# Optimization experiments

Measured on AMD Instinct MI355X. Metric: run time of the kernel, lower is better.

Reference implementation:

```python
import jax, jax.numpy as jnp
import numpy as np

DIM = 1024
NUM_HEAD = 16
DIM_HEAD = DIM // NUM_HEAD
RMS_EPS = 1.1920929e-07  # torch.finfo(float32).eps (nn.RMSNorm default eps=None)
EPS_LIN = 1e-6
THETA = 10000.0


def rmsnorm(x, g, eps=RMS_EPS):
    return x * jax.lax.rsqrt(jnp.mean(x * x, axis=-1, keepdims=True) + eps) * g


def rope_cos_sin(seq_len, dim_head, dtype=jnp.float32):
    inv_freq = 1.0 / (THETA ** (jnp.arange(0, dim_head, 2, dtype=dtype) / dim_head))
    t = jnp.arange(seq_len, dtype=dtype)
    freqs = jnp.outer(t, inv_freq)  # [L, dh//2]
    return jnp.cos(freqs), jnp.sin(freqs)


def apply_rope(t, cos, sin):
    # t: [b, h, L, dh]; pairs are (t[...,2i], t[...,2i+1]) viewed as complex
    tr = t[..., 0::2]
    ti = t[..., 1::2]
    out_r = tr * cos - ti * sin
    out_i = tr * sin + ti * cos
    return jnp.stack([out_r, out_i], axis=-1).reshape(t.shape)


def setup_inputs() -> dict:
    key = jax.random.key(0)
    ks = jax.random.split(key, 5)
    B, L = 4, 4096
    x = jax.random.normal(ks[0], (B, L, DIM), dtype=jnp.float32)
    Wqkv = jax.random.normal(ks[1], (3 * DIM, DIM), dtype=jnp.float32) * 0.02
    bqkv = jax.random.normal(ks[2], (3 * DIM,), dtype=jnp.float32) * 0.02
    gq = jnp.ones((DIM,), dtype=jnp.float32)
    gk = jnp.ones((DIM,), dtype=jnp.float32)
    Wout = jax.random.normal(ks[3], (DIM, DIM), dtype=jnp.float32) * 0.02
    bout = jax.random.normal(ks[4], (DIM,), dtype=jnp.float32) * 0.02
    gout = jnp.ones((DIM,), dtype=jnp.float32)
    return {"x": x, "Wqkv": Wqkv, "bqkv": bqkv, "gq": gq, "gk": gk,
            "Wout": Wout, "bout": bout, "gout": gout}


def reference(x, Wqkv, bqkv, gq, gk, Wout, bout, gout):
    B, L, D = x.shape
    qkv = x @ Wqkv.T + bqkv  # [B, L, 3D]
    q, k, v = jnp.split(qkv, 3, axis=-1)
    q = rmsnorm(q, gq)
    k = rmsnorm(k, gk)
    # b L (h d) -> b h L d
    split = lambda t: t.reshape(B, L, NUM_HEAD, DIM_HEAD).transpose(0, 2, 1, 3)
    q, k, v = split(q), split(k), split(v)
    cos, sin = rope_cos_sin(L, DIM_HEAD)  # start_pos = 0 (default)
    cos = cos[None, None]  # [1,1,L,dh//2]
    sin = sin[None, None]
    q = apply_rope(q, cos, sin)
    k = apply_rope(k, cos, sin)
    # linear attention: ReLU feature map + padded-value normalization trick
    qf = jax.nn.relu(q)
    kf = jax.nn.relu(k)
    vpad = jnp.concatenate([v, jnp.ones_like(v[..., :1])], axis=-1)  # pad_val=1.0
    vk = jnp.einsum('bhlp,bhld->bhpd', vpad, kf)       # [b,h,dh+1,dh]
    res = jnp.einsum('bhpd,bhld->bhlp', vk, qf)        # [b,h,L,dh+1]
    attn = res[..., :-1] / (res[..., -1:] + EPS_LIN)
    attn = attn.transpose(0, 2, 1, 3).reshape(B, L, D)  # b h L d -> b L (h d)
    out = rmsnorm(attn @ Wout.T + bout, gout)
    return out
```

## Files before the change

kernel.cpp:

```cpp
#include <hip/hip_runtime.h>
#include <stdint.h>

#define RMS_EPS 1.1920929e-07f
#define EPS_LIN 1e-6f

typedef __attribute__((ext_vector_type(8))) short bf16x8;
typedef __attribute__((ext_vector_type(4))) float f32x4;

__device__ __forceinline__ unsigned short f2bf(float f) {
  union { float f; unsigned int u; } v; v.f = f;
  unsigned int r = v.u + 0x7fffu + ((v.u >> 16) & 1u);
  return (unsigned short)(r >> 16);
}
__device__ __forceinline__ float bf2f(unsigned short s) {
  union { unsigned int u; float f; } v; v.u = ((unsigned int)s) << 16;
  return v.f;
}

__global__ __launch_bounds__(256) void k_init(
    const float* __restrict__ x, const float* __restrict__ Wqkv,
    const float* __restrict__ Wout,
    unsigned short* __restrict__ xb, unsigned short* __restrict__ wqkvb,
    unsigned short* __restrict__ woutb,
    float* __restrict__ cosT, float* __restrict__ sinT) {
  const int blk = blockIdx.x;
  const int t = threadIdx.x;
  if (blk < 20480) {
    const float* src;
    unsigned short* dst;
    int base;
    if (blk < 16384) { src = x; dst = xb; base = blk; }
    else if (blk < 19456) { src = Wqkv; dst = wqkvb; base = blk - 16384; }
    else { src = Wout; dst = woutb; base = blk - 19456; }
    int i = (base * 256 + t) * 4;
    float4 v = *reinterpret_cast<const float4*>(src + i);
    ushort4 o = { f2bf(v.x), f2bf(v.y), f2bf(v.z), f2bf(v.w) };
    *reinterpret_cast<ushort4*>(dst + i) = o;
  } else {
    int idx = (blk - 20480) * 256 + t;
    int l = idx >> 5, i = idx & 31;
    float inv_freq = expf(-((float)(2 * i) / 64.0f) * logf(10000.0f));
    float ang = (float)l * inv_freq;
    cosT[idx] = cosf(ang);
    sinT[idx] = sinf(ang);
  }
}

__device__ __forceinline__ void stage16(const unsigned short* g, unsigned short* lds_base,
                                        int lane) {
#if __has_builtin(__builtin_amdgcn_global_load_lds)
  __builtin_amdgcn_global_load_lds(
      (const __attribute__((address_space(1))) unsigned int*)g,
      (__attribute__((address_space(3))) unsigned int*)lds_base, 16, 0, 0);
#else
  *reinterpret_cast<uint4*>(lds_base + lane * 8) = *reinterpret_cast<const uint4*>(g);
#endif
}

__global__ __launch_bounds__(256, 3) void k_gemm_bt(
    const unsigned short* __restrict__ A, const unsigned short* __restrict__ Bw,
    const float* __restrict__ bias, int M, int N, int K, int mode,
    unsigned short* __restrict__ qb, unsigned short* __restrict__ kb,
    unsigned short* __restrict__ vb, unsigned short* __restrict__ preb) {
  __shared__ unsigned short As[128 * 64];
  __shared__ unsigned short Bs[128 * 64];
  const int nt = N >> 7;
  const int nwg = gridDim.x;
  const int wg = (blockIdx.x & 7) * (nwg >> 3) + (blockIdx.x >> 3);
  int ksplit = 0, tile = wg;
  if (mode == 1) { ksplit = wg >> 10; tile = wg & 1023; }
  const int bm = tile / nt, bn = tile % nt;
  const int m0 = bm << 7, n0 = bn << 7;
  const int kbeg = (mode == 1) ? (ksplit << 9) : 0;
  const int kend = (mode == 1) ? (kbeg + 512) : K;
  const int t = threadIdx.x;
  const int wave = t >> 6, lane = t & 63;
  const int wr = wave >> 1, wc = wave & 1;
  const int quad = lane >> 4, m16 = lane & 15;

  const unsigned short* ApS[4];
  const unsigned short* BpS[4];
  unsigned short* AlS[4];
  unsigned short* BlS[4];
#pragma unroll
  for (int s = 0; s < 4; ++s) {
    int u = wave * 256 + s * 64 + lane;
    int row = u >> 3;
    int ku = (u & 7) ^ (row & 7);
    ApS[s] = A + (size_t)(m0 + row) * K + ku * 8;
    BpS[s] = Bw + (size_t)(n0 + row) * K + ku * 8;
    AlS[s] = As + (size_t)(wave * 256 + s * 64) * 8;
    BlS[s] = Bs + (size_t)(wave * 256 + s * 64) * 8;
  }

  int offA[4][2], offB[4][2];
#pragma unroll
  for (int i = 0; i < 4; ++i) {
    int rowA = wr * 64 + i * 16 + m16;
    int rowB = wc * 64 + i * 16 + m16;
#pragma unroll
    for (int ks = 0; ks < 2; ++ks) {
      int kuf = ks * 4 + quad;
      offA[i][ks] = (rowA * 8 + (kuf ^ (rowA & 7))) * 8;
      offB[i][ks] = (rowB * 8 + (kuf ^ (rowB & 7))) * 8;
    }
  }

  f32x4 acc[4][4] = {};

  for (int k0 = kbeg; k0 < kend; k0 += 64) {
#pragma unroll
    for (int s = 0; s < 4; ++s) {
      stage16(ApS[s] + k0, AlS[s], lane);
      stage16(BpS[s] + k0, BlS[s], lane);
    }
    __syncthreads();
#pragma unroll
    for (int ks = 0; ks < 2; ++ks) {
      bf16x8 fa[4], fb[4];
#pragma unroll
      for (int i = 0; i < 4; ++i)
        fa[i] = *reinterpret_cast<const bf16x8*>(As + offA[i][ks]);
#pragma unroll
      for (int j = 0; j < 4; ++j)
        fb[j] = *reinterpret_cast<const bf16x8*>(Bs + offB[j][ks]);
#pragma unroll
      for (int i = 0; i < 4; ++i)
#pragma unroll
        for (int j = 0; j < 4; ++j)
          acc[i][j] = __builtin_amdgcn_mfma_f32_16x16x32_bf16(fa[i], fb[j], acc[i][j], 0, 0, 0);
    }
    __syncthreads();
  }

  unsigned short* po = preb + (size_t)ksplit * 16777216ull;
#pragma unroll
  for (int i = 0; i < 4; ++i) {
    int rbase = m0 + wr * 64 + i * 16 + quad * 4;
#pragma unroll
    for (int j = 0; j < 4; ++j) {
      int col = n0 + wc * 64 + j * 16 + m16;
      float bc = (mode == 0 || ksplit == 0) ? bias[col] : 0.f;
#pragma unroll
      for (int r = 0; r < 4; ++r) {
        int row = rbase + r;
        float val = acc[i][j][r] + bc;
        unsigned short bv = f2bf(val);
        if (mode == 0) {
          if (col < 1024) {
            qb[(size_t)row * 1024 + col] = bv;
          } else if (col < 2048) {
            kb[(size_t)row * 1024 + (col - 1024)] = bv;
          } else {
            int h = (col - 2048) >> 6, d = col & 63;
            int b = row >> 12, l = row & 4095;
            vb[(((size_t)(b * 16 + h)) * 4096 + l) * 64 + d] = bv;
          }
        } else {
          po[(size_t)row * N + col] = bv;
        }
      }
    }
  }
}

__global__ __launch_bounds__(256) void k_qknorm(
    const unsigned short* __restrict__ qb, const unsigned short* __restrict__ kb,
    const float* __restrict__ gq, const float* __restrict__ gk,
    const float* __restrict__ cosT, const float* __restrict__ sinT,
    unsigned short* __restrict__ qfb, unsigned short* __restrict__ kfb) {
  const int wid = (blockIdx.x << 2) + (threadIdx.x >> 6);
  const int row = wid >> 1;
  const int which = wid & 1;
  const int lane = threadIdx.x & 63;
  const int l = row & 4095;
  const int b = row >> 12;
  const unsigned short* src = (which ? kb : qb) + (size_t)row * 1024 + lane * 16;
  const float* g = which ? gk : gq;
  unsigned short* dstb = which ? kfb : qfb;

  bf16x8 u0 = *reinterpret_cast<const bf16x8*>(src);
  bf16x8 u1 = *reinterpret_cast<const bf16x8*>(src + 8);
  float v[16];
  float ss = 0.f;
#pragma unroll
  for (int e = 0; e < 8; ++e) {
    v[e] = bf2f((unsigned short)u0[e]);
    v[8 + e] = bf2f((unsigned short)u1[e]);
  }
#pragma unroll
  for (int e = 0; e < 16; ++e) ss += v[e] * v[e];
#pragma unroll
  for (int off = 1; off < 64; off <<= 1) ss += __shfl_xor(ss, off, 64);
  const float sc = rsqrtf(ss * (1.0f / 1024.0f) + RMS_EPS);

  const float* gp = g + lane * 16;
  const float* cp = cosT + l * 32 + (lane & 3) * 8;
  const float* sp = sinT + l * 32 + (lane & 3) * 8;
  bf16x8 o0, o1;
#pragma unroll
  for (int p = 0; p < 8; ++p) {
    float cc = cp[p], sv = sp[p];
    float x0 = v[2 * p] * sc * gp[2 * p];
    float x1 = v[2 * p + 1] * sc * gp[2 * p + 1];
    float r0 = x0 * cc - x1 * sv;
    float r1 = x0 * sv + x1 * cc;
    unsigned short b0 = f2bf(fmaxf(r0, 0.f));
    unsigned short b1 = f2bf(fmaxf(r1, 0.f));
    if (p < 4) { o0[2 * p] = (short)b0; o0[2 * p + 1] = (short)b1; }
    else { o1[2 * (p - 4)] = (short)b0; o1[2 * (p - 4) + 1] = (short)b1; }
  }
  unsigned short* dp =
      dstb + (((size_t)(b * 16 + (lane >> 2))) * 4096 + l) * 64 + (lane & 3) * 16;
  *reinterpret_cast<bf16x8*>(dp) = o0;
  *reinterpret_cast<bf16x8*>(dp + 8) = o1;
}

__global__ __launch_bounds__(256) void k_vk(const unsigned short* __restrict__ vb,
                                            const unsigned short* __restrict__ kfb,
                                            float* __restrict__ part) {
  const int bh = blockIdx.x >> 4;
  const int chunk = blockIdx.x & 15;
  const int t = threadIdx.x;
  const int wv = t >> 6, lane = t & 63;
  const int quad = lane >> 4, m16 = lane & 15;

  __shared__ __align__(16) unsigned short Vt[64 * 40];
  __shared__ __align__(16) unsigned short Kt[64 * 40];
  __shared__ float dred[4][64];

  f32x4 acc[4] = {};
  float accD = 0.f;

  for (int tile = 0; tile < 8; ++tile) {
    const size_t rbase =
        ((size_t)bh * 4096 + chunk * 256 + tile * 32 + wv * 8) * 64 + lane;
    bf16x8 vv, kv;
#pragma unroll
    for (int j = 0; j < 8; ++j) {
      unsigned short ve = vb[rbase + j * 64];
      unsigned short ke = kfb[rbase + j * 64];
      vv[j] = (short)ve;
      kv[j] = (short)ke;
      accD += bf2f(ke);
    }
    *reinterpret_cast<bf16x8*>(Vt + lane * 40 + wv * 8) = vv;
    *reinterpret_cast<bf16x8*>(Kt + lane * 40 + wv * 8) = kv;
    __syncthreads();

    bf16x8 fa = *reinterpret_cast<const bf16x8*>(Vt + (wv * 16 + m16) * 40 + quad * 8);
#pragma unroll
    for (int j = 0; j < 4; ++j) {
      bf16x8 fb = *reinterpret_cast<const bf16x8*>(Kt + (j * 16 + m16) * 40 + quad * 8);
      acc[j] = __builtin_amdgcn_mfma_f32_16x16x32_bf16(fa, fb, acc[j], 0, 0, 0);
    }
    __syncthreads();
  }

  float* dst = part + ((size_t)chunk * 64 + bh) * 4160;
#pragma unroll
  for (int j = 0; j < 4; ++j)
#pragma unroll
    for (int r = 0; r < 4; ++r)
      dst[(wv * 16 + quad * 4 + r) * 64 + j * 16 + m16] = acc[j][r];

  dred[wv][lane] = accD;
  __syncthreads();
  if (t < 64) dst[64 * 64 + t] = dred[0][t] + dred[1][t] + dred[2][t] + dred[3][t];
}

__global__ __launch_bounds__(256) void k_vkred(const float* __restrict__ part,
                                               float* __restrict__ vk) {
  const int i = (blockIdx.x * 256 + threadIdx.x) * 4;
  float4 s = *reinterpret_cast<const float4*>(part + i);
#pragma unroll
  for (int c = 1; c < 16; ++c) {
    float4 r = *reinterpret_cast<const float4*>(part + (size_t)c * 266240 + i);
    s.x += r.x; s.y += r.y; s.z += r.z; s.w += r.w;
  }
  *reinterpret_cast<float4*>(vk + i) = s;
}

__global__ __launch_bounds__(256) void k_res(const unsigned short* __restrict__ qfb,
                                             const float* __restrict__ vk,
                                             unsigned short* __restrict__ attnb) {
  const int bh = blockIdx.x >> 5;
  const int lt = (blockIdx.x & 31) << 7;
  const int b = bh >> 4, h = bh & 15;
  const int t = threadIdx.x;
  const int wave = t >> 6, lane = t & 63;
  __shared__ unsigned short Aq[128 * 64];
  __shared__ unsigned short Bv[64 * 64];
  __shared__ float vkD[64];
  __shared__ float invden[128];

  const unsigned short* Ag = qfb + ((size_t)bh * 4096 + lt) * 64;
#pragma unroll
  for (int s = 0; s < 4; ++s)
    stage16(Ag + wave * 2048 + s * 512 + lane * 8, Aq + wave * 2048 + s * 512, lane);

  const float* vsrc = vk + (size_t)bh * 65 * 64;
  {
    int base = t * 16;
#pragma unroll
    for (int c = 0; c < 4; ++c) {
      float4 f = *reinterpret_cast<const float4*>(vsrc + base + c * 4);
      ushort4 o = { f2bf(f.x), f2bf(f.y), f2bf(f.z), f2bf(f.w) };
      *reinterpret_cast<ushort4*>(Bv + base + c * 4) = o;
    }
  }
  if (t < 64) vkD[t] = vsrc[64 * 64 + t];
  __syncthreads();

  f32x4 acc[2][4] = {};
  const int quad = lane >> 4, m16 = lane & 15;
#pragma unroll
  for (int step = 0; step < 2; ++step) {
    bf16x8 fa[2], fb[4];
#pragma unroll
    for (int i = 0; i < 2; ++i)
      fa[i] = *reinterpret_cast<const bf16x8*>(Aq + (wave * 32 + i * 16 + m16) * 64 +
                                               step * 32 + quad * 8);
#pragma unroll
    for (int j = 0; j < 4; ++j)
      fb[j] = *reinterpret_cast<const bf16x8*>(Bv + (j * 16 + m16) * 64 +
                                               step * 32 + quad * 8);
#pragma unroll
    for (int i = 0; i < 2; ++i)
#pragma unroll
      for (int j = 0; j < 4; ++j)
        acc[i][j] = __builtin_amdgcn_mfma_f32_16x16x32_bf16(fa[i], fb[j], acc[i][j], 0, 0, 0);
  }

  {
    const unsigned short* qr = Aq + (t >> 1) * 64 + (t & 1) * 32;
    const float* vd = vkD + (t & 1) * 32;
    float ds = 0.f;
#pragma unroll
    for (int c = 0; c < 4; ++c) {
      bf16x8 qv = *reinterpret_cast<const bf16x8*>(qr + c * 8);
#pragma unroll
      for (int j = 0; j < 8; ++j)
        ds += bf2f((unsigned short)qv[j]) * vd[c * 8 + j];
    }
    ds += __shfl_xor(ds, 1, 64);
    if ((t & 1) == 0) invden[t >> 1] = 1.0f / (ds + EPS_LIN);
  }
  __syncthreads();

#pragma unroll
  for (int i = 0; i < 2; ++i) {
#pragma unroll
    for (int r = 0; r < 4; ++r) {
      int row = wave * 32 + i * 16 + quad * 4 + r;
      float inv = invden[row];
      unsigned short* dst = attnb + ((size_t)(b * 4096 + lt + row)) * 1024 + h * 64;
#pragma unroll
      for (int j = 0; j < 4; ++j)
        dst[j * 16 + m16] = f2bf(acc[i][j][r] * inv);
    }
  }
}

__global__ __launch_bounds__(256) void k_outnorm(const unsigned short* __restrict__ preb0,
                                                 const unsigned short* __restrict__ preb1,
                                                 const float* __restrict__ gout,
                                                 float* __restrict__ out) {
  const int row = (blockIdx.x << 2) + (threadIdx.x >> 6);
  const int lane = threadIdx.x & 63;
  const unsigned short* s0 = preb0 + (size_t)row * 1024 + lane * 16;
  const unsigned short* s1 = preb1 + (size_t)row * 1024 + lane * 16;
  float* drow = out + (size_t)row * 1024 + lane * 16;
  bf16x8 a0 = *reinterpret_cast<const bf16x8*>(s0);
  bf16x8 a1 = *reinterpret_cast<const bf16x8*>(s0 + 8);
  bf16x8 b0 = *reinterpret_cast<const bf16x8*>(s1);
  bf16x8 b1 = *reinterpret_cast<const bf16x8*>(s1 + 8);
  float v[16];
  float ss = 0.f;
#pragma unroll
  for (int e = 0; e < 8; ++e) {
    v[e] = bf2f((unsigned short)a0[e]) + bf2f((unsigned short)b0[e]);
    v[8 + e] = bf2f((unsigned short)a1[e]) + bf2f((unsigned short)b1[e]);
  }
#pragma unroll
  for (int e = 0; e < 16; ++e) ss += v[e] * v[e];
#pragma unroll
  for (int off = 1; off < 64; off <<= 1) ss += __shfl_xor(ss, off, 64);
  const float sc = rsqrtf(ss * (1.0f / 1024.0f) + RMS_EPS);
  const float* gp = gout + lane * 16;
#pragma unroll
  for (int c = 0; c < 4; ++c) {
    float4 o = { v[c * 4 + 0] * sc * gp[c * 4 + 0], v[c * 4 + 1] * sc * gp[c * 4 + 1],
                 v[c * 4 + 2] * sc * gp[c * 4 + 2], v[c * 4 + 3] * sc * gp[c * 4 + 3] };
    *reinterpret_cast<float4*>(drow + c * 4) = o;
  }
}

#define OFF_XB     0ull
#define OFF_WQKVB  33554432ull
#define OFF_WOUTB  39845888ull
#define OFF_QB     41943040ull
#define OFF_KB     75497472ull
#define OFF_VB     109051904ull
#define OFF_QFB    142606336ull
#define OFF_KFB    176160768ull
#define OFF_VK     209715200ull
#define OFF_ATTNB  210780160ull
#define OFF_COST   244334592ull
#define OFF_SINT   244858880ull
#define WS_NEEDED  245383168ull

extern "C" void kernel_launch(void* const* d_in, const int* in_sizes, int n_in,
                              void* d_out, int out_size, void* d_ws, size_t ws_size,
                              hipStream_t stream) {
  const float* x    = (const float*)d_in[0];
  const float* Wqkv = (const float*)d_in[1];
  const float* bqkv = (const float*)d_in[2];
  const float* gq   = (const float*)d_in[3];
  const float* gk   = (const float*)d_in[4];
  const float* Wout = (const float*)d_in[5];
  const float* bout = (const float*)d_in[6];
  const float* gout = (const float*)d_in[7];

  if (ws_size < WS_NEEDED) return;

  char* ws = (char*)d_ws;
  unsigned short* xb    = (unsigned short*)(ws + OFF_XB);
  unsigned short* wqkvb = (unsigned short*)(ws + OFF_WQKVB);
  unsigned short* woutb = (unsigned short*)(ws + OFF_WOUTB);
  unsigned short* qb    = (unsigned short*)(ws + OFF_QB);
  unsigned short* kb    = (unsigned short*)(ws + OFF_KB);
  unsigned short* vb    = (unsigned short*)(ws + OFF_VB);
  unsigned short* qfb   = (unsigned short*)(ws + OFF_QFB);
  unsigned short* kfb   = (unsigned short*)(ws + OFF_KFB);
  float*          vkbuf = (float*)(ws + OFF_VK);
  unsigned short* attnb = (unsigned short*)(ws + OFF_ATTNB);
  float*          cosT  = (float*)(ws + OFF_COST);
  float*          sinT  = (float*)(ws + OFF_SINT);
  unsigned short* preb0 = (unsigned short*)(ws + OFF_QB);
  unsigned short* preb1 = (unsigned short*)(ws + OFF_KB);
  float*          vkpart = (float*)(ws + OFF_ATTNB);

  k_init<<<20992, 256, 0, stream>>>(x, Wqkv, Wout, xb, wqkvb, woutb, cosT, sinT);

  k_gemm_bt<<<128 * 24, 256, 0, stream>>>(xb, wqkvb, bqkv, 16384, 3072, 1024, 0,
                                          qb, kb, vb, nullptr);
  k_qknorm<<<8192, 256, 0, stream>>>(qb, kb, gq, gk, cosT, sinT, qfb, kfb);

  k_vk<<<1024, 256, 0, stream>>>(vb, kfb, vkpart);
  k_vkred<<<260, 256, 0, stream>>>(vkpart, vkbuf);

  k_res<<<2048, 256, 0, stream>>>(qfb, vkbuf, attnb);

  k_gemm_bt<<<2048, 256, 0, stream>>>(attnb, woutb, bout, 16384, 1024, 1024, 1,
                                      nullptr, nullptr, nullptr, preb0);
  k_outnorm<<<4096, 256, 0, stream>>>(preb0, preb1, gout, (float*)d_out);
}
```

Before: 386.1 us.

## Fuse x fp32-to-bf16 conversion into QKV GEMM and drop out-proj split-K

The QKV GEMM now reads x directly in fp32 and converts to bf16 while staging into LDS, removing the separate conversion pass over x and the bf16 copy it wrote. The output-projection GEMM drops its 2-way split-K, writing one pre-norm buffer, so the norm kernel reads one partial instead of summing two. The blockIdx swizzle for L2 locality is also removed. In exchange, the QKV GEMM does synchronous fp32 loads (twice the bytes) instead of async global_load_lds, and the out GEMM launches half as many workgroups.

After: 438.3 us. 1.14x slower.

```diff
diff --git a/kernel.cpp b/kernel.cpp
--- a/kernel.cpp
+++ b/kernel.cpp
@@ -18,26 +18,23 @@
 }
 
 __global__ __launch_bounds__(256) void k_init(
-    const float* __restrict__ x, const float* __restrict__ Wqkv,
-    const float* __restrict__ Wout,
-    unsigned short* __restrict__ xb, unsigned short* __restrict__ wqkvb,
-    unsigned short* __restrict__ woutb,
+    const float* __restrict__ Wqkv, const float* __restrict__ Wout,
+    unsigned short* __restrict__ wqkvb, unsigned short* __restrict__ woutb,
     float* __restrict__ cosT, float* __restrict__ sinT) {
   const int blk = blockIdx.x;
   const int t = threadIdx.x;
-  if (blk < 20480) {
+  if (blk < 4096) {
     const float* src;
     unsigned short* dst;
     int base;
-    if (blk < 16384) { src = x; dst = xb; base = blk; }
-    else if (blk < 19456) { src = Wqkv; dst = wqkvb; base = blk - 16384; }
-    else { src = Wout; dst = woutb; base = blk - 19456; }
+    if (blk < 3072) { src = Wqkv; dst = wqkvb; base = blk; }
+    else { src = Wout; dst = woutb; base = blk - 3072; }
     int i = (base * 256 + t) * 4;
     float4 v = *reinterpret_cast<const float4*>(src + i);
     ushort4 o = { f2bf(v.x), f2bf(v.y), f2bf(v.z), f2bf(v.w) };
     *reinterpret_cast<ushort4*>(dst + i) = o;
   } else {
-    int idx = (blk - 20480) * 256 + t;
+    int idx = (blk - 4096) * 256 + t;
     int l = idx >> 5, i = idx & 31;
     float inv_freq = expf(-((float)(2 * i) / 64.0f) * logf(10000.0f));
     float ang = (float)l * inv_freq;
@@ -58,26 +55,22 @@
 }
 
 __global__ __launch_bounds__(256, 3) void k_gemm_bt(
-    const unsigned short* __restrict__ A, const unsigned short* __restrict__ Bw,
+    const float* __restrict__ Af, const unsigned short* __restrict__ A,
+    const unsigned short* __restrict__ Bw,
     const float* __restrict__ bias, int M, int N, int K, int mode,
     unsigned short* __restrict__ qb, unsigned short* __restrict__ kb,
     unsigned short* __restrict__ vb, unsigned short* __restrict__ preb) {
   __shared__ unsigned short As[128 * 64];
   __shared__ unsigned short Bs[128 * 64];
   const int nt = N >> 7;
-  const int nwg = gridDim.x;
-  const int wg = (blockIdx.x & 7) * (nwg >> 3) + (blockIdx.x >> 3);
-  int ksplit = 0, tile = wg;
-  if (mode == 1) { ksplit = wg >> 10; tile = wg & 1023; }
-  const int bm = tile / nt, bn = tile % nt;
+  const int bm = blockIdx.x / nt, bn = blockIdx.x % nt;
   const int m0 = bm << 7, n0 = bn << 7;
-  const int kbeg = (mode == 1) ? (ksplit << 9) : 0;
-  const int kend = (mode == 1) ? (kbeg + 512) : K;
   const int t = threadIdx.x;
   const int wave = t >> 6, lane = t & 63;
   const int wr = wave >> 1, wc = wave & 1;
   const int quad = lane >> 4, m16 = lane & 15;
 
+  const float* AfS[4];
   const unsigned short* ApS[4];
   const unsigned short* BpS[4];
   unsigned short* AlS[4];
@@ -87,6 +80,7 @@
     int u = wave * 256 + s * 64 + lane;
     int row = u >> 3;
     int ku = (u & 7) ^ (row & 7);
+    AfS[s] = Af + (size_t)(m0 + row) * K + ku * 8;
     ApS[s] = A + (size_t)(m0 + row) * K + ku * 8;
     BpS[s] = Bw + (size_t)(n0 + row) * K + ku * 8;
     AlS[s] = As + (size_t)(wave * 256 + s * 64) * 8;
@@ -108,11 +102,27 @@
 
   f32x4 acc[4][4] = {};
 
-  for (int k0 = kbeg; k0 < kend; k0 += 64) {
-#pragma unroll
-    for (int s = 0; s < 4; ++s) {
-      stage16(ApS[s] + k0, AlS[s], lane);
-      stage16(BpS[s] + k0, BlS[s], lane);
+  for (int k0 = 0; k0 < K; k0 += 64) {
+    if (mode == 0) {
+#pragma unroll
+      for (int s = 0; s < 4; ++s) {
+        const float* p = AfS[s] + k0;
+        float4 f0 = *reinterpret_cast<const float4*>(p);
+        float4 f1 = *reinterpret_cast<const float4*>(p + 4);
+        bf16x8 o;
+        o[0] = (short)f2bf(f0.x); o[1] = (short)f2bf(f0.y);
+        o[2] = (short)f2bf(f0.z); o[3] = (short)f2bf(f0.w);
+        o[4] = (short)f2bf(f1.x); o[5] = (short)f2bf(f1.y);
+        o[6] = (short)f2bf(f1.z); o[7] = (short)f2bf(f1.w);
+        *reinterpret_cast<bf16x8*>(AlS[s] + lane * 8) = o;
+        stage16(BpS[s] + k0, BlS[s], lane);
+      }
+    } else {
+#pragma unroll
+      for (int s = 0; s < 4; ++s) {
+        stage16(ApS[s] + k0, AlS[s], lane);
+        stage16(BpS[s] + k0, BlS[s], lane);
+      }
     }
     __syncthreads();
 #pragma unroll
@@ -133,14 +143,13 @@
     __syncthreads();
   }
 
-  unsigned short* po = preb + (size_t)ksplit * 16777216ull;
 #pragma unroll
   for (int i = 0; i < 4; ++i) {
     int rbase = m0 + wr * 64 + i * 16 + quad * 4;
 #pragma unroll
     for (int j = 0; j < 4; ++j) {
       int col = n0 + wc * 64 + j * 16 + m16;
-      float bc = (mode == 0 || ksplit == 0) ? bias[col] : 0.f;
+      float bc = bias[col];
 #pragma unroll
       for (int r = 0; r < 4; ++r) {
         int row = rbase + r;
@@ -157,7 +166,7 @@
             vb[(((size_t)(b * 16 + h)) * 4096 + l) * 64 + d] = bv;
           }
         } else {
-          po[(size_t)row * N + col] = bv;
+          preb[(size_t)row * N + col] = bv;
         }
       }
     }
@@ -362,25 +371,21 @@
   }
 }
 
-__global__ __launch_bounds__(256) void k_outnorm(const unsigned short* __restrict__ preb0,
-                                                 const unsigned short* __restrict__ preb1,
+__global__ __launch_bounds__(256) void k_outnorm(const unsigned short* __restrict__ preb,
                                                  const float* __restrict__ gout,
                                                  float* __restrict__ out) {
   const int row = (blockIdx.x << 2) + (threadIdx.x >> 6);
   const int lane = threadIdx.x & 63;
-  const unsigned short* s0 = preb0 + (size_t)row * 1024 + lane * 16;
-  const unsigned short* s1 = preb1 + (size_t)row * 1024 + lane * 16;
+  const unsigned short* src = preb + (size_t)row * 1024 + lane * 16;
   float* drow = out + (size_t)row * 1024 + lane * 16;
-  bf16x8 a0 = *reinterpret_cast<const bf16x8*>(s0);
-  bf16x8 a1 = *reinterpret_cast<const bf16x8*>(s0 + 8);
-  bf16x8 b0 = *reinterpret_cast<const bf16x8*>(s1);
-  bf16x8 b1 = *reinterpret_cast<const bf16x8*>(s1 + 8);
+  bf16x8 a0 = *reinterpret_cast<const bf16x8*>(src);
+  bf16x8 a1 = *reinterpret_cast<const bf16x8*>(src + 8);
   float v[16];
   float ss = 0.f;
 #pragma unroll
   for (int e = 0; e < 8; ++e) {
-    v[e] = bf2f((unsigned short)a0[e]) + bf2f((unsigned short)b0[e]);
-    v[8 + e] = bf2f((unsigned short)a1[e]) + bf2f((unsigned short)b1[e]);
+    v[e] = bf2f((unsigned short)a0[e]);
+    v[8 + e] = bf2f((unsigned short)a1[e]);
   }
 #pragma unroll
   for (int e = 0; e < 16; ++e) ss += v[e] * v[e];
@@ -425,7 +430,6 @@
   if (ws_size < WS_NEEDED) return;
 
   char* ws = (char*)d_ws;
-  unsigned short* xb    = (unsigned short*)(ws + OFF_XB);
   unsigned short* wqkvb = (unsigned short*)(ws + OFF_WQKVB);
   unsigned short* woutb = (unsigned short*)(ws + OFF_WOUTB);
   unsigned short* qb    = (unsigned short*)(ws + OFF_QB);
@@ -437,13 +441,12 @@
   unsigned short* attnb = (unsigned short*)(ws + OFF_ATTNB);
   float*          cosT  = (float*)(ws + OFF_COST);
   float*          sinT  = (float*)(ws + OFF_SINT);
-  unsigned short* preb0 = (unsigned short*)(ws + OFF_QB);
-  unsigned short* preb1 = (unsigned short*)(ws + OFF_KB);
+  unsigned short* preb  = (unsigned short*)(ws + OFF_QB);
   float*          vkpart = (float*)(ws + OFF_ATTNB);
 
-  k_init<<<20992, 256, 0, stream>>>(x, Wqkv, Wout, xb, wqkvb, woutb, cosT, sinT);
-
-  k_gemm_bt<<<128 * 24, 256, 0, stream>>>(xb, wqkvb, bqkv, 16384, 3072, 1024, 0,
+  k_init<<<4608, 256, 0, stream>>>(Wqkv, Wout, wqkvb, woutb, cosT, sinT);
+
+  k_gemm_bt<<<128 * 24, 256, 0, stream>>>(x, nullptr, wqkvb, bqkv, 16384, 3072, 1024, 0,
                                           qb, kb, vb, nullptr);
   k_qknorm<<<8192, 256, 0, stream>>>(qb, kb, gq, gk, cosT, sinT, qfb, kfb);
 
@@ -452,7 +455,7 @@
 
   k_res<<<2048, 256, 0, stream>>>(qfb, vkbuf, attnb);
 
-  k_gemm_bt<<<2048, 256, 0, stream>>>(attnb, woutb, bout, 16384, 1024, 1024, 1,
-                                      nullptr, nullptr, nullptr, preb0);
-  k_outnorm<<<4096, 256, 0, stream>>>(preb0, preb1, gout, (float*)d_out);
-}
+  k_gemm_bt<<<128 * 8, 256, 0, stream>>>(nullptr, attnb, woutb, bout, 16384, 1024, 1024, 1,
+                                         nullptr, nullptr, nullptr, preb);
+  k_outnorm<<<4096, 256, 0, stream>>>(preb, gout, (float*)d_out);
+}
```

## Drop split-K in output GEMM, remove XCD swizzle, raise occupancy hint

Applied to the files above, without the earlier changes.

Removes the two-way split-K in the output projection GEMM, so each workgroup now computes the full K=1024 reduction and writes a single bf16 pre-norm buffer. The outnorm kernel then reads one partial instead of summing two. This drops a second 32MB bf16 partial write and read and one extra rounding step. In exchange the output GEMM launches only 1024 workgroups, fewer than before. The change also removes the XCD-aware block remapping and raises the launch_bounds occupancy hint from 3 to 4 waves per SIMD, which may restrict registers.

Result: faster. 374.1 us (median of 2 runs) (-3.1%).

```diff
diff --git a/kernel.cpp b/kernel.cpp
--- a/kernel.cpp
+++ b/kernel.cpp
@@ -57,7 +57,7 @@
 #endif
 }
 
-__global__ __launch_bounds__(256, 3) void k_gemm_bt(
+__global__ __launch_bounds__(256, 4) void k_gemm_bt(
     const unsigned short* __restrict__ A, const unsigned short* __restrict__ Bw,
     const float* __restrict__ bias, int M, int N, int K, int mode,
     unsigned short* __restrict__ qb, unsigned short* __restrict__ kb,
@@ -65,14 +65,8 @@
   __shared__ unsigned short As[128 * 64];
   __shared__ unsigned short Bs[128 * 64];
   const int nt = N >> 7;
-  const int nwg = gridDim.x;
-  const int wg = (blockIdx.x & 7) * (nwg >> 3) + (blockIdx.x >> 3);
-  int ksplit = 0, tile = wg;
-  if (mode == 1) { ksplit = wg >> 10; tile = wg & 1023; }
-  const int bm = tile / nt, bn = tile % nt;
+  const int bm = blockIdx.x / nt, bn = blockIdx.x % nt;
   const int m0 = bm << 7, n0 = bn << 7;
-  const int kbeg = (mode == 1) ? (ksplit << 9) : 0;
-  const int kend = (mode == 1) ? (kbeg + 512) : K;
   const int t = threadIdx.x;
   const int wave = t >> 6, lane = t & 63;
   const int wr = wave >> 1, wc = wave & 1;
@@ -108,7 +102,7 @@
 
   f32x4 acc[4][4] = {};
 
-  for (int k0 = kbeg; k0 < kend; k0 += 64) {
+  for (int k0 = 0; k0 < K; k0 += 64) {
 #pragma unroll
     for (int s = 0; s < 4; ++s) {
       stage16(ApS[s] + k0, AlS[s], lane);
@@ -133,14 +127,13 @@
     __syncthreads();
   }
 
-  unsigned short* po = preb + (size_t)ksplit * 16777216ull;
 #pragma unroll
   for (int i = 0; i < 4; ++i) {
     int rbase = m0 + wr * 64 + i * 16 + quad * 4;
 #pragma unroll
     for (int j = 0; j < 4; ++j) {
       int col = n0 + wc * 64 + j * 16 + m16;
-      float bc = (mode == 0 || ksplit == 0) ? bias[col] : 0.f;
+      float bc = bias[col];
 #pragma unroll
       for (int r = 0; r < 4; ++r) {
         int row = rbase + r;
@@ -157,7 +150,7 @@
             vb[(((size_t)(b * 16 + h)) * 4096 + l) * 64 + d] = bv;
           }
         } else {
-          po[(size_t)row * N + col] = bv;
+          preb[(size_t)row * N + col] = bv;
         }
       }
     }
@@ -362,25 +355,21 @@
   }
 }
 
-__global__ __launch_bounds__(256) void k_outnorm(const unsigned short* __restrict__ preb0,
-                                                 const unsigned short* __restrict__ preb1,
+__global__ __launch_bounds__(256) void k_outnorm(const unsigned short* __restrict__ preb,
                                                  const float* __restrict__ gout,
                                                  float* __restrict__ out) {
   const int row = (blockIdx.x << 2) + (threadIdx.x >> 6);
   const int lane = threadIdx.x & 63;
-  const unsigned short* s0 = preb0 + (size_t)row * 1024 + lane * 16;
-  const unsigned short* s1 = preb1 + (size_t)row * 1024 + lane * 16;
+  const unsigned short* src = preb + (size_t)row * 1024 + lane * 16;
   float* drow = out + (size_t)row * 1024 + lane * 16;
-  bf16x8 a0 = *reinterpret_cast<const bf16x8*>(s0);
-  bf16x8 a1 = *reinterpret_cast<const bf16x8*>(s0 + 8);
-  bf16x8 b0 = *reinterpret_cast<const bf16x8*>(s1);
-  bf16x8 b1 = *reinterpret_cast<const bf16x8*>(s1 + 8);
+  bf16x8 a0 = *reinterpret_cast<const bf16x8*>(src);
+  bf16x8 a1 = *reinterpret_cast<const bf16x8*>(src + 8);
   float v[16];
   float ss = 0.f;
 #pragma unroll
   for (int e = 0; e < 8; ++e) {
-    v[e] = bf2f((unsigned short)a0[e]) + bf2f((unsigned short)b0[e]);
-    v[8 + e] = bf2f((unsigned short)a1[e]) + bf2f((unsigned short)b1[e]);
+    v[e] = bf2f((unsigned short)a0[e]);
+    v[8 + e] = bf2f((unsigned short)a1[e]);
   }
 #pragma unroll
   for (int e = 0; e < 16; ++e) ss += v[e] * v[e];
@@ -437,8 +426,7 @@
   unsigned short* attnb = (unsigned short*)(ws + OFF_ATTNB);
   float*          cosT  = (float*)(ws + OFF_COST);
   float*          sinT  = (float*)(ws + OFF_SINT);
-  unsigned short* preb0 = (unsigned short*)(ws + OFF_QB);
-  unsigned short* preb1 = (unsigned short*)(ws + OFF_KB);
+  unsigned short* preb  = (unsigned short*)(ws + OFF_QB);
   float*          vkpart = (float*)(ws + OFF_ATTNB);
 
   k_init<<<20992, 256, 0, stream>>>(x, Wqkv, Wout, xb, wqkvb, woutb, cosT, sinT);
@@ -452,7 +440,7 @@
 
   k_res<<<2048, 256, 0, stream>>>(qfb, vkbuf, attnb);
 
-  k_gemm_bt<<<2048, 256, 0, stream>>>(attnb, woutb, bout, 16384, 1024, 1024, 1,
-                                      nullptr, nullptr, nullptr, preb0);
-  k_outnorm<<<4096, 256, 0, stream>>>(preb0, preb1, gout, (float*)d_out);
-}
+  k_gemm_bt<<<128 * 8, 256, 0, stream>>>(attnb, woutb, bout, 16384, 1024, 1024, 1,
+                                         nullptr, nullptr, nullptr, preb);
+  k_outnorm<<<4096, 256, 0, stream>>>(preb, gout, (float*)d_out);
+}
```
